# Kernel tuning notes

Measured on AMD Instinct MI355X. Metric: run time of the kernel, lower is better.

## Reference

```python
import jax, jax.numpy as jnp
import numpy as np

B, S, NH, D_IN = 64, 512, 4, 256   # batch, seq_len, rnn n_head, input_dim
H = 256                            # hidden_dim == attention activation_dim
AH = 256                           # attention_hidden_dim (attn out_dim)
OUT = 3                            # output_dim (sentiment classes)


def setup_inputs() -> dict:
    key = jax.random.key(0)
    ks = jax.random.split(key, 9)
    def p(k, shape, scale=0.05):
        return jax.random.normal(k, shape, dtype=jnp.float32) * scale
    return dict(
        x=jax.random.normal(ks[0], (B, S, NH, D_IN), dtype=jnp.float32),
        Wk=p(ks[1], (D_IN, H)), bk=jnp.zeros((H,), jnp.float32),
        Wq=p(ks[2], (H, H)),    bq=jnp.zeros((H,), jnp.float32),
        w_mlp=p(ks[3], (2 * H,)),
        Wproj=p(ks[4], (H, AH)), bproj=jnp.zeros((AH,), jnp.float32),
        W1=p(ks[5], (D_IN + AH, H)), b1=jnp.zeros((H,), jnp.float32),
        W2=p(ks[6], (H, H)),    b2=jnp.zeros((H,), jnp.float32),
        Wo=p(ks[7], (NH * H, OUT)), bo=jnp.zeros((OUT,), jnp.float32),
    )


def _cell(x_t, hidden, params):
    Wk, bk, Wq, bq, w_mlp, Wproj, bproj, W1, b1, W2, b2, Wo, bo = params
    kx = x_t @ Wk + bk           # [B, NH, H]  keys from step input
    qx = hidden @ Wq + bq        # [B, NH, H]  queries from hidden state
    w1, w2 = w_mlp[:H], w_mlp[H:]
    # MLP score: s[b,i,j] = tanh(cat(kx[b,j], qx[b,i]) . w) = tanh(kx[b,j].w1 + qx[b,i].w2)
    score = jnp.tanh((qx @ w2)[:, :, None] + (kx @ w1)[:, None, :])  # [B, NH, NH]
    score = jax.nn.softmax(score, axis=-1)
    attn = jnp.einsum('bij,bjh->bih', score, kx) @ Wproj + bproj     # [B, NH, AH]
    concat = jnp.concatenate([x_t, attn], axis=-1)                   # [B, NH, D_IN+AH]
    hidden_new = jax.nn.relu(concat @ W1 + b1) @ W2 + b2             # [B, NH, H]
    logits = hidden_new.reshape(B, NH * H) @ Wo + bo                 # [B, OUT]
    out = jax.nn.log_softmax(logits, axis=-1)
    return out, hidden_new


def reference(x, Wk, bk, Wq, bq, w_mlp, Wproj, bproj, W1, b1, W2, b2, Wo, bo):
    params = (Wk, bk, Wq, bq, w_mlp, Wproj, bproj, W1, b1, W2, b2, Wo, bo)
    h0 = jnp.zeros((B, NH, H), x.dtype)
    xs = jnp.swapaxes(x, 0, 1)  # [S, B, NH, D_IN] for scan over time
    def step(h, x_t):
        out, h_new = _cell(x_t, h, params)
        return h_new, out
    h_final, outs = jax.lax.scan(step, h0, xs)
    # return_sequence=False: last-step log-softmax output and final hidden
    return outs[-1], h_final
```

## Files before the change

kernel.cpp:

```cpp
#include <hip/hip_runtime.h>
#include <hip/hip_bf16.h>
#include <math.h>

#define BB   64
#define SS   512
#define NHH  4
#define DD   256
#define HH   256
#define LDH  264

typedef __attribute__((ext_vector_type(8))) short  short8;
typedef __attribute__((ext_vector_type(4))) float  floatx4;


__device__ __forceinline__ unsigned short f2b(float f) {
  __hip_bfloat16 h = __float2bfloat16(f);
  return __builtin_bit_cast(unsigned short, h);
}
__device__ __forceinline__ float b2f(unsigned short u) {
  unsigned v = (unsigned)u << 16;
  return __builtin_bit_cast(float, v);
}

__global__ __launch_bounds__(256) void init_kernel(
    const float* __restrict__ Wk, const float* __restrict__ Wproj,
    const float* __restrict__ W1, const float* __restrict__ Wq,
    const float* __restrict__ bq, const float* __restrict__ w_mlp,
    const float* __restrict__ bproj, const float* __restrict__ W2,
    const float* __restrict__ b2, float* __restrict__ ws,
    unsigned short* __restrict__ wpack)
{
  __shared__ float vsh[256];
  __shared__ float red[256];
  int tid = threadIdx.x;

  if (blockIdx.x > 0) {
    int idx = (blockIdx.x - 1) * 256 + tid;
    int mat = idx >> 16;
    int rem = idx & 65535;
    int j    = rem & 7;
    int lane = (rem >> 3) & 63;
    int ks   = (rem >> 9) & 7;
    int pan  = rem >> 12;
    int k = ks * 32 + ((lane >> 4) << 3) + j;
    int n = pan * 16 + (lane & 15);
    float v;
    if      (mat == 0) v = Wk[k * 256 + n];
    else if (mat == 1) v = W1[k * 256 + n];
    else if (mat == 2) v = Wproj[k * 256 + n];
    else               v = W1[(256 + k) * 256 + n];
    wpack[idx] = f2b(v);
    return;
  }

  const float* w2 = w_mlp + HH;
  {
    float a = 0.f;
    const float4* Wq4 = (const float4*)(Wq + tid * 256);
    const float4* w24 = (const float4*)w2;
    for (int k = 0; k < 64; ++k) {
      float4 wv = Wq4[k], xv = w24[k];
      a = fmaf(wv.x, xv.x, fmaf(wv.y, xv.y, fmaf(wv.z, xv.z, fmaf(wv.w, xv.w, a))));
    }
    vsh[tid] = a;
  }
  __syncthreads();
  {
    float a2 = 0.f;
    const float4* W24 = (const float4*)(W2 + tid * 256);
    const float4* v4  = (const float4*)vsh;
    for (int k = 0; k < 64; ++k) {
      float4 wv = W24[k], xv = v4[k];
      a2 = fmaf(wv.x, xv.x, fmaf(wv.y, xv.y, fmaf(wv.z, xv.z, fmaf(wv.w, xv.w, a2))));
    }
    ws[tid] = a2;
  }
  {
    float a3 = 0.f;
    for (int k = 0; k < 256; ++k) a3 = fmaf(bproj[k], W1[(256 + k) * 256 + tid], a3);
    ws[256 + tid] = a3;
  }
  red[tid] = bq[tid] * w2[tid];
  __syncthreads();
  for (int s = 128; s; s >>= 1) { if (tid < s) red[tid] += red[tid + s]; __syncthreads(); }
  float c = red[0];
  __syncthreads();
  ws[768 + tid] = c;
  red[tid] = b2[tid] * vsh[tid];
  __syncthreads();
  for (int s = 128; s; s >>= 1) { if (tid < s) red[tid] += red[tid + s]; __syncthreads(); }
  if (tid == 0) ws[512] = red[0] + c;
}

__device__ __forceinline__ void mfma_gemm4(
    const unsigned short* A_lds, const short8* __restrict__ Bp,
    const float* __restrict__ bias, floatx4 acc[4][4], int l, int w)
{
  int col = l & 15, quad = l >> 4;
#pragma unroll
  for (int pp = 0; pp < 4; ++pp) {
    float bv = bias ? bias[(w * 4 + pp) * 16 + col] : 0.f;
#pragma unroll
    for (int mf = 0; mf < 4; ++mf)
      acc[mf][pp] = (floatx4){bv, bv, bv, bv};
  }
  const short8* Bb = Bp + (size_t)(w * 4) * 512 + l;
  short8 bb[3][4];
  short8 aa[2][4];
#pragma unroll
  for (int pp = 0; pp < 4; ++pp) bb[0][pp] = Bb[pp * 512];
#pragma unroll
  for (int pp = 0; pp < 4; ++pp) bb[1][pp] = Bb[pp * 512 + 64];
#pragma unroll
  for (int mf = 0; mf < 4; ++mf)
    aa[0][mf] = *(const short8*)(A_lds + (mf * 16 + col) * LDH + quad * 8);
#pragma unroll
  for (int kb = 0; kb < 8; ++kb) {
    if (kb + 2 < 8) {
#pragma unroll
      for (int pp = 0; pp < 4; ++pp)
        bb[(kb + 2) % 3][pp] = Bb[pp * 512 + (kb + 2) * 64];
    }
    if (kb + 1 < 8) {
#pragma unroll
      for (int mf = 0; mf < 4; ++mf)
        aa[(kb + 1) & 1][mf] =
            *(const short8*)(A_lds + (mf * 16 + col) * LDH + (kb + 1) * 32 + quad * 8);
    }
#pragma unroll
    for (int mf = 0; mf < 4; ++mf)
#pragma unroll
      for (int pp = 0; pp < 4; ++pp)
        acc[mf][pp] = __builtin_amdgcn_mfma_f32_16x16x32_bf16(
            aa[kb & 1][mf], bb[kb % 3][pp], acc[mf][pp], 0, 0, 0);
  }
}

__device__ __forceinline__ void acc_to_lds(
    unsigned short* D, const floatx4 acc[4][4], int l, int w)
{
  int col = l & 15, quad = l >> 4;
#pragma unroll
  for (int mf = 0; mf < 4; ++mf)
#pragma unroll
    for (int pp = 0; pp < 4; ++pp)
#pragma unroll
      for (int r = 0; r < 4; ++r)
        D[(mf * 16 + quad * 4 + r) * LDH + (w * 4 + pp) * 16 + col] = f2b(acc[mf][pp][r]);
}

__device__ __forceinline__ void acc_to_global(
    unsigned short* __restrict__ dst, const floatx4 acc[4][4],
    int l, int w, int b, int tt)
{
  int col = l & 15, quad = l >> 4;
#pragma unroll
  for (int mf = 0; mf < 4; ++mf)
#pragma unroll
    for (int r = 0; r < 4; ++r) {
      int m2 = mf * 16 + quad * 4 + r;
      size_t base = (((size_t)(tt * 16 + (m2 >> 2)) * 64 + b) * 4 + (m2 & 3)) * 256;
#pragma unroll
      for (int pp = 0; pp < 4; ++pp)
        dst[base + (w * 4 + pp) * 16 + col] = f2b(acc[mf][pp][r]);
    }
}

__device__ void precompute_block(
    int px, const float* __restrict__ x, const unsigned short* __restrict__ wpack,
    const float* __restrict__ bk, const float* __restrict__ b1,
    const float* __restrict__ w_mlp,
    float* __restrict__ kw_c, unsigned short* __restrict__ xw1_c,
    unsigned short* __restrict__ kpw_c, int t0, char* smem)
{
  float* kwbuf = (float*)smem;
  unsigned short* XS = (unsigned short*)(smem + 2048);
  unsigned short* TS = XS + 64 * LDH;

  int b  = px & 63;
  int tt = px >> 6;
  int tid = threadIdx.x;
  int l = tid & 63, w = tid >> 6;
  int col = l & 15, quad = l >> 4;

  const float4* xsrc = (const float4*)(x + (size_t)(b * SS + t0 + tt * 16) * NHH * DD);
#pragma unroll
  for (int i = 0; i < 16; ++i) {
    int f4 = i * 256 + tid;
    int r = f4 >> 6, c4 = f4 & 63;
    float4 v = xsrc[f4];
    ushort4 h;
    h.x = f2b(v.x); h.y = f2b(v.y); h.z = f2b(v.z); h.w = f2b(v.w);
    *(ushort4*)&XS[r * LDH + c4 * 4] = h;
  }
  __syncthreads();

  const short8* wp0 = (const short8*)(wpack);
  const short8* wp1 = (const short8*)(wpack + 65536);
  const short8* wp2 = (const short8*)(wpack + 2 * 65536);
  const short8* wp3 = (const short8*)(wpack + 3 * 65536);

  floatx4 acc[4][4];

  mfma_gemm4(XS, wp0, bk, acc, l, w);
  acc_to_lds(TS, acc, l, w);
  __syncthreads();

  {
    float part = 0.f;
    const unsigned short* trow = TS + l * LDH + w * 64;
#pragma unroll
    for (int j8 = 0; j8 < 8; ++j8) {
      short8 tv = *(const short8*)(trow + j8 * 8);
#pragma unroll
      for (int j = 0; j < 8; ++j)
        part = fmaf(b2f((unsigned short)tv[j]), w_mlp[w * 64 + j8 * 8 + j], part);
    }
    kwbuf[l * 4 + w] = part;
  }

  mfma_gemm4(XS, wp1, b1, acc, l, w);
  __syncthreads();
  if (tid < 64) {
    float s = kwbuf[tid * 4] + kwbuf[tid * 4 + 1] + kwbuf[tid * 4 + 2] + kwbuf[tid * 4 + 3];
    kw_c[((size_t)(tt * 16 + (tid >> 2)) * 64 + b) * 4 + (tid & 3)] = s;
  }
  acc_to_global(xw1_c, acc, l, w, b, tt);

  mfma_gemm4(TS, wp2, nullptr, acc, l, w);
  acc_to_lds(XS, acc, l, w);
  __syncthreads();

  mfma_gemm4(XS, wp3, nullptr, acc, l, w);
  acc_to_global(kpw_c, acc, l, w, b, tt);
}

__device__ __forceinline__ float wave_reduce_sum(float x) {
#define DPPSTEP(ctrl, rmask)                                                   \
  {                                                                            \
    int _s = __builtin_amdgcn_update_dpp(0, __builtin_bit_cast(int, x),        \
                                         (ctrl), (rmask), 0xf, true);          \
    x += __builtin_bit_cast(float, _s);                                        \
  }
  DPPSTEP(0x111, 0xf)
  DPPSTEP(0x112, 0xf)
  DPPSTEP(0x114, 0xf)
  DPPSTEP(0x118, 0xf)
  DPPSTEP(0x142, 0xa)
  DPPSTEP(0x143, 0xc)
#undef DPPSTEP
  return __builtin_bit_cast(float, __builtin_amdgcn_readlane(__builtin_bit_cast(int, x), 63));
}

__device__ __forceinline__ float tanh_fast(float y) {
  float ex = __expf(2.f * y);
  return 1.f - 2.f * __builtin_amdgcn_rcpf(ex + 1.f);
}

__device__ void seq_block(
    const unsigned short* __restrict__ xw1_c, const unsigned short* __restrict__ kpw_c,
    const float* __restrict__ kw_c, float* __restrict__ ws,
    float* __restrict__ relu_u, int t0, int n)
{
  int b = blockIdx.x;
  int tid = threadIdx.x;
  int i = tid >> 6, l = tid & 63;

  float4 v2v = ((const float4*)ws)[l];
  float4 cbv = ((const float4*)(ws + 256))[l];
  float c2 = ws[512];
  float qw = ws[768 + b * 4 + i];

  const ushort4* xw = (const ushort4*)xw1_c;
  const ushort4* kp = (const ushort4*)kpw_c;

  struct Slot { ushort4 x, k0, k1, k2, k3; float4 kw; };

  auto load = [&](Slot& s, int tc) {
    size_t rb_ = (size_t)(tc * 64 + b) * 4;
    s.x  = xw[(rb_ + i) * 64 + l];
    s.k0 = kp[(rb_ + 0) * 64 + l];
    s.k1 = kp[(rb_ + 1) * 64 + l];
    s.k2 = kp[(rb_ + 2) * 64 + l];
    s.k3 = kp[(rb_ + 3) * 64 + l];
    s.kw = *(const float4*)&kw_c[rb_];
  };

  auto step = [&](Slot& s, int t) {
    float e0 = tanh_fast(qw + s.kw.x);
    float e1 = tanh_fast(qw + s.kw.y);
    float e2 = tanh_fast(qw + s.kw.z);
    float e3 = tanh_fast(qw + s.kw.w);
    float q0 = __expf(e0), q1 = __expf(e1), q2 = __expf(e2), q3 = __expf(e3);
    float inv = __builtin_amdgcn_rcpf(q0 + q1 + q2 + q3);
    float4 K0 = {b2f(s.k0.x), b2f(s.k0.y), b2f(s.k0.z), b2f(s.k0.w)};
    float4 K1 = {b2f(s.k1.x), b2f(s.k1.y), b2f(s.k1.z), b2f(s.k1.w)};
    float4 K2 = {b2f(s.k2.x), b2f(s.k2.y), b2f(s.k2.z), b2f(s.k2.w)};
    float4 K3 = {b2f(s.k3.x), b2f(s.k3.y), b2f(s.k3.z), b2f(s.k3.w)};
    float4 X  = {b2f(s.x.x) + cbv.x, b2f(s.x.y) + cbv.y,
                 b2f(s.x.z) + cbv.z, b2f(s.x.w) + cbv.w};
    float4 a;
    a.x = fmaf(q0, K0.x, fmaf(q1, K1.x, fmaf(q2, K2.x, q3 * K3.x)));
    a.y = fmaf(q0, K0.y, fmaf(q1, K1.y, fmaf(q2, K2.y, q3 * K3.y)));
    a.z = fmaf(q0, K0.z, fmaf(q1, K1.z, fmaf(q2, K2.z, q3 * K3.z)));
    a.w = fmaf(q0, K0.w, fmaf(q1, K1.w, fmaf(q2, K2.w, q3 * K3.w)));
    float4 u;
    u.x = fmaf(a.x, inv, X.x); u.y = fmaf(a.y, inv, X.y);
    u.z = fmaf(a.z, inv, X.z); u.w = fmaf(a.w, inv, X.w);
    float4 r;
    r.x = fmaxf(u.x, 0.f); r.y = fmaxf(u.y, 0.f);
    r.z = fmaxf(u.z, 0.f); r.w = fmaxf(u.w, 0.f);
    float d = fmaf(r.x, v2v.x, fmaf(r.y, v2v.y, fmaf(r.z, v2v.z, r.w * v2v.w)));
    qw = wave_reduce_sum(d) + c2;
    if (t0 + t == SS - 1)
      *(float4*)&relu_u[(size_t)(b * 4 + i) * 256 + l * 4] = r;
  };

  Slot s0, s1, s2, s3;
  load(s0, 0); load(s1, 1); load(s2, 2); load(s3, 3);
  for (int t = 0; t < n; t += 4) {
    int nt;
    step(s0, t);     nt = t + 4; load(s0, nt < n ? nt : n - 1);
    step(s1, t + 1); nt = t + 5; load(s1, nt < n ? nt : n - 1);
    step(s2, t + 2); nt = t + 6; load(s2, nt < n ? nt : n - 1);
    step(s3, t + 3); nt = t + 7; load(s3, nt < n ? nt : n - 1);
  }
  if (l == 0) ws[768 + b * 4 + i] = qw;
}

__global__ __launch_bounds__(256, 2) void fused_kernel(
    const float* __restrict__ x, const unsigned short* __restrict__ wpack,
    const float* __restrict__ bk, const float* __restrict__ b1,
    const float* __restrict__ w_mlp,
    float* kwB, unsigned short* xw1B, unsigned short* kpwB, int t0_pre,
    const float* kwA, const unsigned short* xw1A, const unsigned short* kpwA,
    int t0_seq, int n_seq,
    float* __restrict__ ws, float* __restrict__ relu_u)
{
  __shared__ __align__(16) char smem[2048 + 2 * 64 * LDH * 2];
  if (blockIdx.x < 64) {
    if (n_seq > 0) seq_block(xw1A, kpwA, kwA, ws, relu_u, t0_seq, n_seq);
    return;
  }
  precompute_block(blockIdx.x - 64, x, wpack, bk, b1, w_mlp,
                   kwB, xw1B, kpwB, t0_pre, smem);
}

__global__ __launch_bounds__(256) void final_hidden_kernel(
    const float* __restrict__ relu_u, const float* __restrict__ W2,
    const float* __restrict__ b2, float* __restrict__ out)
{
  __shared__ float rs[256];
  int row = blockIdx.x;
  int tid = threadIdx.x;
  rs[tid] = relu_u[(size_t)row * 256 + tid];
  __syncthreads();
  float acc = b2[tid];
  for (int k = 0; k < 256; ++k) acc = fmaf(rs[k], W2[k * 256 + tid], acc);
  out[192 + (size_t)row * 256 + tid] = acc;
}

__global__ __launch_bounds__(256) void final_logits_kernel(
    const float* __restrict__ hf, const float* __restrict__ Wo,
    const float* __restrict__ bo, float* __restrict__ outp)
{
  __shared__ float r0[256], r1[256], r2[256];
  int b = blockIdx.x;
  int tid = threadIdx.x;
  float a0 = 0.f, a1 = 0.f, a2 = 0.f;
  for (int k = tid; k < 1024; k += 256) {
    float h = hf[(size_t)b * 1024 + k];
    a0 = fmaf(h, Wo[k * 3 + 0], a0);
    a1 = fmaf(h, Wo[k * 3 + 1], a1);
    a2 = fmaf(h, Wo[k * 3 + 2], a2);
  }
  r0[tid] = a0; r1[tid] = a1; r2[tid] = a2;
  __syncthreads();
  for (int s = 128; s; s >>= 1) {
    if (tid < s) { r0[tid] += r0[tid + s]; r1[tid] += r1[tid + s]; r2[tid] += r2[tid + s]; }
    __syncthreads();
  }
  if (tid == 0) {
    float l0 = r0[0] + bo[0], l1 = r1[0] + bo[1], l2 = r2[0] + bo[2];
    float m = fmaxf(l0, fmaxf(l1, l2));
    float lse = m + logf(expf(l0 - m) + expf(l1 - m) + expf(l2 - m));
    outp[b * 3 + 0] = l0 - lse;
    outp[b * 3 + 1] = l1 - lse;
    outp[b * 3 + 2] = l2 - lse;
  }
}

extern "C" void kernel_launch(void* const* d_in, const int* in_sizes, int n_in,
                              void* d_out, int out_size, void* d_ws, size_t ws_size,
                              hipStream_t stream)
{
  const float* x     = (const float*)d_in[0];
  const float* Wk    = (const float*)d_in[1];
  const float* bk    = (const float*)d_in[2];
  const float* Wq    = (const float*)d_in[3];
  const float* bq    = (const float*)d_in[4];
  const float* w_mlp = (const float*)d_in[5];
  const float* Wproj = (const float*)d_in[6];
  const float* bproj = (const float*)d_in[7];
  const float* W1    = (const float*)d_in[8];
  const float* b1    = (const float*)d_in[9];
  const float* W2    = (const float*)d_in[10];
  const float* b2    = (const float*)d_in[11];
  const float* Wo    = (const float*)d_in[12];
  const float* bo    = (const float*)d_in[13];
  float* out = (float*)d_out;
  float* ws  = (float*)d_ws;

  float* ru = ws + 1024;
  unsigned short* wpack = (unsigned short*)(ws + 66560);
  const size_t OFF_CH = 66560 + 131072;
  const long per_t = 256 + 65536;

  long ws_floats = (long)(ws_size / 4);
  long avail = ws_floats - (long)OFF_CH;

  int Tc = 128;
  while (Tc > 0 && 2L * Tc * per_t > avail) Tc -= 16;
  bool pipelined = (Tc >= 16);
  if (!pipelined) {
    Tc = 128;
    while (Tc > 16 && (long)Tc * per_t > avail) Tc -= 16;
  }

  float* bufA = ws + OFF_CH;
  float* bufB = pipelined ? bufA + (size_t)Tc * per_t : bufA;

  auto kw_of  = [&](float* base) { return base; };
  auto xw_of  = [&](float* base) { return (unsigned short*)(base + (size_t)Tc * 256); };
  auto kpw_of = [&](float* base) { return (unsigned short*)(base + (size_t)Tc * 256) + (size_t)Tc * 65536; };

  init_kernel<<<1025, 256, 0, stream>>>(Wk, Wproj, W1, Wq, bq, w_mlp, bproj, W2, b2,
                                        ws, wpack);

  int C = (SS + Tc - 1) / Tc;

  if (pipelined) {
    for (int r = 0; r <= C; ++r) {
      bool hasPre = (r < C);
      bool hasSeq = (r >= 1);
      int t0p = r * Tc;
      int np  = hasPre ? ((SS - t0p) < Tc ? (SS - t0p) : Tc) : 0;
      int t0s = (r - 1) * Tc;
      int ns  = hasSeq ? ((SS - t0s) < Tc ? (SS - t0s) : Tc) : 0;
      float* pB = ((r & 1) ? bufB : bufA);
      float* pA = (((r - 1) & 1) ? bufB : bufA);
      int grid = 64 + (hasPre ? 64 * (np / 16) : 0);
      fused_kernel<<<grid, 256, 0, stream>>>(
          x, wpack, bk, b1, w_mlp,
          kw_of(pB), xw_of(pB), kpw_of(pB), t0p,
          kw_of(pA), xw_of(pA), kpw_of(pA), t0s, ns,
          ws, ru);
    }
  } else {
    for (int c = 0; c < C; ++c) {
      int t0 = c * Tc;
      int n = (SS - t0) < Tc ? (SS - t0) : Tc;
      fused_kernel<<<64 + 64 * (n / 16), 256, 0, stream>>>(
          x, wpack, bk, b1, w_mlp,
          kw_of(bufA), xw_of(bufA), kpw_of(bufA), t0,
          kw_of(bufA), xw_of(bufA), kpw_of(bufA), 0, 0,
          ws, ru);
      fused_kernel<<<64, 256, 0, stream>>>(
          x, wpack, bk, b1, w_mlp,
          kw_of(bufA), xw_of(bufA), kpw_of(bufA), t0,
          kw_of(bufA), xw_of(bufA), kpw_of(bufA), t0, n,
          ws, ru);
    }
  }

  final_hidden_kernel<<<BB * NHH, 256, 0, stream>>>(ru, W2, b2, out);
  final_logits_kernel<<<BB, 256, 0, stream>>>(out + 192, Wo, bo, out);
}
```

Before: 427.0 us.

## Fold Wk·Wproj·W1b weight chain into one precomputed matrix

The key projection, attention projection and the attention half of W1 are all linear, so their product Wk·Wproj·W1b is precomputed once in new init kernels, along with Wk·w1 and the folded bias terms. The per-chunk precompute then runs two MFMA GEMMs straight from the bf16 input tile instead of four chained GEMMs with LDS round-trips, and halves shared memory. The cost is two extra setup kernels and different rounding, since the fused matrix is rounded to bf16 once instead of the intermediates being rounded.

```diff
diff --git a/kernel.cpp b/kernel.cpp
--- a/kernel.cpp
+++ b/kernel.cpp
@@ -22,74 +22,118 @@
   return __builtin_bit_cast(float, v);
 }
 
-__global__ __launch_bounds__(256) void init_kernel(
+__global__ __launch_bounds__(256) void init1_kernel(
     const float* __restrict__ Wk, const float* __restrict__ Wproj,
     const float* __restrict__ W1, const float* __restrict__ Wq,
     const float* __restrict__ bq, const float* __restrict__ w_mlp,
-    const float* __restrict__ bproj, const float* __restrict__ W2,
-    const float* __restrict__ b2, float* __restrict__ ws,
-    unsigned short* __restrict__ wpack)
+    const float* __restrict__ W2, const float* __restrict__ b2,
+    const float* __restrict__ bk,
+    float* __restrict__ ws, unsigned short* __restrict__ wpack)
 {
   __shared__ float vsh[256];
   __shared__ float red[256];
   int tid = threadIdx.x;
-
-  if (blockIdx.x > 0) {
-    int idx = (blockIdx.x - 1) * 256 + tid;
-    int mat = idx >> 16;
-    int rem = idx & 65535;
-    int j    = rem & 7;
-    int lane = (rem >> 3) & 63;
-    int ks   = (rem >> 9) & 7;
-    int pan  = rem >> 12;
+  int b = blockIdx.x;
+
+  if (b == 0) {
+    const float* w2 = w_mlp + HH;
+    {
+      float a = 0.f;
+      const float4* Wq4 = (const float4*)(Wq + tid * 256);
+      const float4* w24 = (const float4*)w2;
+      for (int k = 0; k < 64; ++k) {
+        float4 wv = Wq4[k], xv = w24[k];
+        a = fmaf(wv.x, xv.x, fmaf(wv.y, xv.y, fmaf(wv.z, xv.z, fmaf(wv.w, xv.w, a))));
+      }
+      vsh[tid] = a;
+    }
+    __syncthreads();
+    {
+      float a2 = 0.f;
+      const float4* W24 = (const float4*)(W2 + tid * 256);
+      const float4* v4  = (const float4*)vsh;
+      for (int k = 0; k < 64; ++k) {
+        float4 wv = W24[k], xv = v4[k];
+        a2 = fmaf(wv.x, xv.x, fmaf(wv.y, xv.y, fmaf(wv.z, xv.z, fmaf(wv.w, xv.w, a2))));
+      }
+      ws[tid] = a2;
+    }
+    red[tid] = bq[tid] * w_mlp[HH + tid];
+    __syncthreads();
+    for (int s = 128; s; s >>= 1) { if (tid < s) red[tid] += red[tid + s]; __syncthreads(); }
+    float c = red[0];
+    __syncthreads();
+    ws[768 + tid] = c;
+    red[tid] = b2[tid] * vsh[tid];
+    __syncthreads();
+    for (int s = 128; s; s >>= 1) { if (tid < s) red[tid] += red[tid + s]; __syncthreads(); }
+    if (tid == 0) ws[512] = red[0] + c;
+    __syncthreads();
+    red[tid] = bk[tid] * w_mlp[tid];
+    __syncthreads();
+    for (int s = 128; s; s >>= 1) { if (tid < s) red[tid] += red[tid + s]; __syncthreads(); }
+    if (tid == 0) ws[513] = red[0];
+    return;
+  }
+
+  if (b <= 256) {
+    int idx = (b - 1) * 256 + tid;
+    int j    = idx & 7;
+    int lane = (idx >> 3) & 63;
+    int ks   = (idx >> 9) & 7;
+    int pan  = idx >> 12;
     int k = ks * 32 + ((lane >> 4) << 3) + j;
     int n = pan * 16 + (lane & 15);
-    float v;
-    if      (mat == 0) v = Wk[k * 256 + n];
-    else if (mat == 1) v = W1[k * 256 + n];
-    else if (mat == 2) v = Wproj[k * 256 + n];
-    else               v = W1[(256 + k) * 256 + n];
-    wpack[idx] = f2b(v);
+    wpack[idx] = f2b(W1[k * 256 + n]);
     return;
   }
 
-  const float* w2 = w_mlp + HH;
   {
-    float a = 0.f;
-    const float4* Wq4 = (const float4*)(Wq + tid * 256);
-    const float4* w24 = (const float4*)w2;
-    for (int k = 0; k < 64; ++k) {
-      float4 wv = Wq4[k], xv = w24[k];
-      a = fmaf(wv.x, xv.x, fmaf(wv.y, xv.y, fmaf(wv.z, xv.z, fmaf(wv.w, xv.w, a))));
-    }
-    vsh[tid] = a;
-  }
-  __syncthreads();
+    int r = b - 257;
+    const float* w1b = W1 + 256 * 256;
+    float acc = 0.f;
+    for (int k = 0; k < 256; ++k)
+      acc = fmaf(Wproj[r * 256 + k], w1b[k * 256 + tid], acc);
+    ws[132096 + r * 256 + tid] = acc;
+  }
+}
+
+__global__ __launch_bounds__(256) void init2_kernel(
+    const float* __restrict__ Wk, const float* __restrict__ W1,
+    const float* __restrict__ bproj, const float* __restrict__ bk,
+    const float* __restrict__ w_mlp,
+    float* __restrict__ ws, unsigned short* __restrict__ wpack)
+{
+  __shared__ float red[256];
+  int tid = threadIdx.x;
+  int b = blockIdx.x;
+  const float* Wc = ws + 132096;
+
+  if (b < 256) {
+    int r = b;
+    float acc = 0.f;
+    for (int k = 0; k < 256; ++k)
+      acc = fmaf(Wk[r * 256 + k], Wc[k * 256 + tid], acc);
+    int n = tid;
+    int pan = n >> 4, ks = r >> 5, j = r & 7;
+    int lane = ((r >> 3) & 3) * 16 + (n & 15);
+    wpack[65536 + pan * 4096 + ks * 512 + lane * 8 + j] = f2b(acc);
+    red[tid] = Wk[r * 256 + tid] * w_mlp[tid];
+    __syncthreads();
+    for (int s = 128; s; s >>= 1) { if (tid < s) red[tid] += red[tid + s]; __syncthreads(); }
+    if (tid == 0) ws[197632 + r] = red[0];
+    return;
+  }
+
   {
-    float a2 = 0.f;
-    const float4* W24 = (const float4*)(W2 + tid * 256);
-    const float4* v4  = (const float4*)vsh;
-    for (int k = 0; k < 64; ++k) {
-      float4 wv = W24[k], xv = v4[k];
-      a2 = fmaf(wv.x, xv.x, fmaf(wv.y, xv.y, fmaf(wv.z, xv.z, fmaf(wv.w, xv.w, a2))));
-    }
-    ws[tid] = a2;
-  }
-  {
+    const float* w1b = W1 + 256 * 256;
     float a3 = 0.f;
-    for (int k = 0; k < 256; ++k) a3 = fmaf(bproj[k], W1[(256 + k) * 256 + tid], a3);
+    for (int k = 0; k < 256; ++k)
+      a3 = fmaf(bproj[k], w1b[k * 256 + tid], a3);
+    for (int k = 0; k < 256; ++k)
+      a3 = fmaf(bk[k], Wc[k * 256 + tid], a3);
     ws[256 + tid] = a3;
   }
-  red[tid] = bq[tid] * w2[tid];
-  __syncthreads();
-  for (int s = 128; s; s >>= 1) { if (tid < s) red[tid] += red[tid + s]; __syncthreads(); }
-  float c = red[0];
-  __syncthreads();
-  ws[768 + tid] = c;
-  red[tid] = b2[tid] * vsh[tid];
-  __syncthreads();
-  for (int s = 128; s; s >>= 1) { if (tid < s) red[tid] += red[tid + s]; __syncthreads(); }
-  if (tid == 0) ws[512] = red[0] + c;
 }
 
 __device__ __forceinline__ void mfma_gemm4(
@@ -136,19 +180,6 @@
   }
 }
 
-__device__ __forceinline__ void acc_to_lds(
-    unsigned short* D, const floatx4 acc[4][4], int l, int w)
-{
-  int col = l & 15, quad = l >> 4;
-#pragma unroll
-  for (int mf = 0; mf < 4; ++mf)
-#pragma unroll
-    for (int pp = 0; pp < 4; ++pp)
-#pragma unroll
-      for (int r = 0; r < 4; ++r)
-        D[(mf * 16 + quad * 4 + r) * LDH + (w * 4 + pp) * 16 + col] = f2b(acc[mf][pp][r]);
-}
-
 __device__ __forceinline__ void acc_to_global(
     unsigned short* __restrict__ dst, const floatx4 acc[4][4],
     int l, int w, int b, int tt)
@@ -168,20 +199,17 @@
 
 __device__ void precompute_block(
     int px, const float* __restrict__ x, const unsigned short* __restrict__ wpack,
-    const float* __restrict__ bk, const float* __restrict__ b1,
-    const float* __restrict__ w_mlp,
+    const float* __restrict__ b1, const float* __restrict__ ws,
     float* __restrict__ kw_c, unsigned short* __restrict__ xw1_c,
     unsigned short* __restrict__ kpw_c, int t0, char* smem)
 {
   float* kwbuf = (float*)smem;
   unsigned short* XS = (unsigned short*)(smem + 2048);
-  unsigned short* TS = XS + 64 * LDH;
 
   int b  = px & 63;
   int tt = px >> 6;
   int tid = threadIdx.x;
   int l = tid & 63, w = tid >> 6;
-  int col = l & 15, quad = l >> 4;
 
   const float4* xsrc = (const float4*)(x + (size_t)(b * SS + t0 + tt * 16) * NHH * DD);
 #pragma unroll
@@ -195,44 +223,37 @@
   }
   __syncthreads();
 
-  const short8* wp0 = (const short8*)(wpack);
-  const short8* wp1 = (const short8*)(wpack + 65536);
-  const short8* wp2 = (const short8*)(wpack + 2 * 65536);
-  const short8* wp3 = (const short8*)(wpack + 3 * 65536);
-
-  floatx4 acc[4][4];
-
-  mfma_gemm4(XS, wp0, bk, acc, l, w);
-  acc_to_lds(TS, acc, l, w);
-  __syncthreads();
+  const short8* wpA = (const short8*)(wpack);
+  const short8* wpD = (const short8*)(wpack + 65536);
 
   {
+    const float* wkw = ws + 197632;
     float part = 0.f;
-    const unsigned short* trow = TS + l * LDH + w * 64;
+    const unsigned short* trow = XS + l * LDH + w * 64;
 #pragma unroll
     for (int j8 = 0; j8 < 8; ++j8) {
       short8 tv = *(const short8*)(trow + j8 * 8);
 #pragma unroll
       for (int j = 0; j < 8; ++j)
-        part = fmaf(b2f((unsigned short)tv[j]), w_mlp[w * 64 + j8 * 8 + j], part);
+        part = fmaf(b2f((unsigned short)tv[j]), wkw[w * 64 + j8 * 8 + j], part);
     }
     kwbuf[l * 4 + w] = part;
   }
 
-  mfma_gemm4(XS, wp1, b1, acc, l, w);
+  floatx4 acc[4][4];
+
+  mfma_gemm4(XS, wpA, b1, acc, l, w);
+  acc_to_global(xw1_c, acc, l, w, b, tt);
+
+  mfma_gemm4(XS, wpD, nullptr, acc, l, w);
+  acc_to_global(kpw_c, acc, l, w, b, tt);
+
   __syncthreads();
   if (tid < 64) {
-    float s = kwbuf[tid * 4] + kwbuf[tid * 4 + 1] + kwbuf[tid * 4 + 2] + kwbuf[tid * 4 + 3];
+    float s = kwbuf[tid * 4] + kwbuf[tid * 4 + 1] + kwbuf[tid * 4 + 2] + kwbuf[tid * 4 + 3]
+            + ws[513];
     kw_c[((size_t)(tt * 16 + (tid >> 2)) * 64 + b) * 4 + (tid & 3)] = s;
   }
-  acc_to_global(xw1_c, acc, l, w, b, tt);
-
-  mfma_gemm4(TS, wp2, nullptr, acc, l, w);
-  acc_to_lds(XS, acc, l, w);
-  __syncthreads();
-
-  mfma_gemm4(XS, wp3, nullptr, acc, l, w);
-  acc_to_global(kpw_c, acc, l, w, b, tt);
 }
 
 __device__ __forceinline__ float wave_reduce_sum(float x) {
@@ -330,19 +351,18 @@
 
 __global__ __launch_bounds__(256, 2) void fused_kernel(
     const float* __restrict__ x, const unsigned short* __restrict__ wpack,
-    const float* __restrict__ bk, const float* __restrict__ b1,
-    const float* __restrict__ w_mlp,
+    const float* __restrict__ b1,
     float* kwB, unsigned short* xw1B, unsigned short* kpwB, int t0_pre,
     const float* kwA, const unsigned short* xw1A, const unsigned short* kpwA,
     int t0_seq, int n_seq,
     float* __restrict__ ws, float* __restrict__ relu_u)
 {
-  __shared__ __align__(16) char smem[2048 + 2 * 64 * LDH * 2];
+  __shared__ __align__(16) char smem[2048 + 64 * LDH * 2];
   if (blockIdx.x < 64) {
     if (n_seq > 0) seq_block(xw1A, kpwA, kwA, ws, relu_u, t0_seq, n_seq);
     return;
   }
-  precompute_block(blockIdx.x - 64, x, wpack, bk, b1, w_mlp,
+  precompute_block(blockIdx.x - 64, x, wpack, b1, ws,
                    kwB, xw1B, kpwB, t0_pre, smem);
 }
 
@@ -413,7 +433,7 @@
 
   float* ru = ws + 1024;
   unsigned short* wpack = (unsigned short*)(ws + 66560);
-  const size_t OFF_CH = 66560 + 131072;
+  const size_t OFF_CH = 197888;
   const long per_t = 256 + 65536;
 
   long ws_floats = (long)(ws_size / 4);
@@ -434,8 +454,9 @@
   auto xw_of  = [&](float* base) { return (unsigned short*)(base + (size_t)Tc * 256); };
   auto kpw_of = [&](float* base) { return (unsigned short*)(base + (size_t)Tc * 256) + (size_t)Tc * 65536; };
 
-  init_kernel<<<1025, 256, 0, stream>>>(Wk, Wproj, W1, Wq, bq, w_mlp, bproj, W2, b2,
+  init1_kernel<<<513, 256, 0, stream>>>(Wk, Wproj, W1, Wq, bq, w_mlp, W2, b2, bk,
                                         ws, wpack);
+  init2_kernel<<<257, 256, 0, stream>>>(Wk, W1, bproj, bk, w_mlp, ws, wpack);
 
   int C = (SS + Tc - 1) / Tc;
 
@@ -451,7 +472,7 @@
       float* pA = (((r - 1) & 1) ? bufB : bufA);
       int grid = 64 + (hasPre ? 64 * (np / 16) : 0);
       fused_kernel<<<grid, 256, 0, stream>>>(
-          x, wpack, bk, b1, w_mlp,
+          x, wpack, b1,
           kw_of(pB), xw_of(pB), kpw_of(pB), t0p,
           kw_of(pA), xw_of(pA), kpw_of(pA), t0s, ns,
           ws, ru);
@@ -461,12 +482,12 @@
       int t0 = c * Tc;
       int n = (SS - t0) < Tc ? (SS - t0) : Tc;
       fused_kernel<<<64 + 64 * (n / 16), 256, 0, stream>>>(
-          x, wpack, bk, b1, w_mlp,
+          x, wpack, b1,
           kw_of(bufA), xw_of(bufA), kpw_of(bufA), t0,
           kw_of(bufA), xw_of(bufA), kpw_of(bufA), 0, 0,
           ws, ru);
       fused_kernel<<<64, 256, 0, stream>>>(
-          x, wpack, bk, b1, w_mlp,
+          x, wpack, b1,
           kw_of(bufA), xw_of(bufA), kpw_of(bufA), t0,
           kw_of(bufA), xw_of(bufA), kpw_of(bufA), t0, n,
           ws, ru);
```

New measurement: 436.6 us. +2.3%, slower.
